# Performance work log

Measured on AMD Instinct MI355X. Metric: run time of the kernel, lower is better.

Reference implementation:

```python
import jax, jax.numpy as jnp
import numpy as np

C = 64
K = 16
DEPTH = 4            # int(sqrt(K))
N_NODES = K - 1      # 15 internal nodes per subspace tree
D = 512              # input feature dim, D // C = 8 per subspace
M = 512              # output dim (LUT rows)
N = 16384            # number of input rows


def _make_selection_matrix(C, depth=DEPTH):
    # row i within a subspace selects the transformed dim used at tree level of node i
    lvl = [0, 1, 1, 2, 2, 2, 2, 3, 3, 3, 3, 3, 3, 3, 3]
    S = np.zeros((C * N_NODES, C * depth), np.float32)
    for c in range(C):
        for i in range(N_NODES):
            S[c * N_NODES + i, c * depth + lvl[i]] = 1.0
    return S


def _make_bit_matrix(C, K=K):
    # per-subspace (K, K-1) matrix: leaf k gets +/-1 on the 4 nodes along its root-to-leaf path
    Bm = np.zeros((K, N_NODES), np.float32)
    for k in range(K):
        node = 0
        for l in range(DEPTH):
            bit = (k >> (DEPTH - 1 - l)) & 1
            Bm[k, node] = 1.0 if bit else -1.0
            node = 2 * node + 1 + bit  # children of node i are 2i+1 (left) and 2i+2 (right)
    Bfull = np.zeros((C * K, C * N_NODES), np.float32)
    for c in range(C):
        Bfull[c * K:(c + 1) * K, c * N_NODES:(c + 1) * N_NODES] = Bm
    return Bfull


def setup_inputs() -> dict:
    key = jax.random.key(0)
    k1, k2, k3, k4 = jax.random.split(key, 4)
    I = jax.random.normal(k1, (N, D), dtype=jnp.float32)
    A = jax.random.normal(k2, (C, D // C, DEPTH), dtype=jnp.float32) * (1.0 / np.sqrt(D // C))
    T = jax.random.normal(k3, (C * N_NODES,), dtype=jnp.float32) * 0.1
    L = jax.random.normal(k4, (M, C, K), dtype=jnp.float32)
    S = jnp.asarray(_make_selection_matrix(C))
    B = jnp.asarray(_make_bit_matrix(C))
    return {"I": I, "A": A, "T": T, "L": L, "S": S, "B": B}


def reference(I, A, T, L, S, B):
    C_, sub, depth = A.shape
    Kq = L.shape[-1]
    n = I.shape[0]
    # block-diagonal per-subspace projection: (n, D) -> (n, C*depth)
    Ir = I.T.reshape(C_, sub, n)                      # (C, sub, n)
    xt = jnp.einsum('csn,csd->cdn', Ir, A)            # (C, depth, n)
    xt = xt.reshape(C_ * depth, n)                    # (C*depth, n)
    # tree encoding: per-node activations, tanh relaxation, leaf scores
    h = S @ xt - T[:, None]                           # (C*15, n)
    b = (B @ jnp.tanh(h)).reshape(C_, Kq, n)          # (C, K, n)
    # straight-through hard one-hot encoding with softmax backward
    E_soft = jax.nn.softmax(b, axis=1)
    E_hard = jax.nn.one_hot(jnp.argmax(b, axis=1), Kq, axis=1, dtype=b.dtype)
    E = E_hard + E_soft - jax.lax.stop_gradient(E_soft)  # (C, K, n)
    # LUT decode: out[n, m] = sum_c L[m, c, enc(n, c)]
    out = jnp.einsum('mck,ckn->nm', L, E)
    return out
```

## Files before the change

### kernel.cpp

```cpp
#include <hip/hip_runtime.h>
#include <hip/hip_fp16.h>
#include <math.h>

#define CC 64
#define KK 16
#define NNODES 15
#define DD 512
#define MM 512
#define NN 16384

__device__ __forceinline__ float xla_tanhf(float x) {
    const float kMax = 7.90531110763549805f;
    bool tiny = fabsf(x) < 0.0004f;
    float xc = fminf(fmaxf(x, -kMax), kMax);
    float x2 = __fmul_rn(xc, xc);
    float p = __fmaf_rn(x2, -2.76076847742355e-16f, 2.00018790482477e-13f);
    p = __fmaf_rn(x2, p, -8.60467152213735e-11f);
    p = __fmaf_rn(x2, p, 5.12229709037114e-08f);
    p = __fmaf_rn(x2, p, 1.48572235717979e-05f);
    p = __fmaf_rn(x2, p, 6.37261928875436e-04f);
    p = __fmaf_rn(x2, p, 4.89352455891786e-03f);
    p = __fmul_rn(xc, p);
    float q = __fmaf_rn(x2, 1.19825839466702e-06f, 1.18534705686654e-04f);
    q = __fmaf_rn(x2, q, 2.26843463243900e-03f);
    q = __fmaf_rn(x2, q, 4.89352518554385e-03f);
    return tiny ? x : __fdiv_rn(p, q);
}

__global__ __launch_bounds__(256) void transpose_lut16(const float* __restrict__ L,
                                                       __half* __restrict__ Lt) {
    __shared__ __half tile[64 * 72];
    const int tid = threadIdx.x;
    const int ck0 = (blockIdx.x & 15) * 64;
    const int m0  = (blockIdx.x >> 4) * 64;

    const int col = tid & 63;
#pragma unroll
    for (int i = 0; i < 16; ++i) {
        int r = (tid >> 6) + i * 4;
        float v = L[(size_t)(m0 + r) * (CC * KK) + ck0 + col];
        tile[col * 72 + r] = __float2half(v);
    }
    __syncthreads();

#pragma unroll
    for (int t = 0; t < 2; ++t) {
        int cr   = (tid >> 3) + t * 32;
        int mseg = (tid & 7) * 8;
        uint4 v = *(const uint4*)&tile[cr * 72 + mseg];
        *(uint4*)(Lt + ((size_t)(ck0 + cr) * MM + m0 + mseg)) = v;
    }
}

__global__ __launch_bounds__(256) void fused_kernel(const float* __restrict__ I,
                                                    const float* __restrict__ A,
                                                    const float* __restrict__ T,
                                                    const __half* __restrict__ Lt,
                                                    float* __restrict__ out) {
    __shared__ float sA[CC * 8 * 4];
    __shared__ float sT[CC * NNODES];
    __shared__ unsigned char sIdx[4 * CC];

    const int tid = threadIdx.x;
    for (int i = tid; i < CC * 32; i += 256) sA[i] = A[i];
    for (int i = tid; i < CC * NNODES; i += 256) sT[i] = T[i];
    __syncthreads();

    const int w    = tid >> 6;
    const int lane = tid & 63;
    const int c    = lane;
    const int j    = blockIdx.x * 4 + w;

    {
        const float* Ij = I + (size_t)j * DD + c * 8;
        float4 v0 = ((const float4*)Ij)[0];
        float4 v1 = ((const float4*)Ij)[1];
        float iv[8] = {v0.x, v0.y, v0.z, v0.w, v1.x, v1.y, v1.z, v1.w};

        float t[4] = {0.f, 0.f, 0.f, 0.f};
#pragma unroll
        for (int s = 0; s < 8; ++s) {
            float v = iv[s];
#pragma unroll
            for (int d = 0; d < 4; ++d)
                t[d] = __fmaf_rn(v, sA[c * 32 + s * 4 + d], t[d]);
        }

        const int lvl[NNODES] = {0, 1, 1, 2, 2, 2, 2, 3, 3, 3, 3, 3, 3, 3, 3};
        float th[NNODES];
#pragma unroll
        for (int i = 0; i < NNODES; ++i) {
            float h = __fsub_rn(t[lvl[i]], sT[c * NNODES + i]);
            th[i] = xla_tanhf(h);
        }

        int best = 0;
        float bestv = -3.0e38f;
#pragma unroll
        for (int k = 0; k < KK; ++k) {
            int node = 0;
            float s = 0.f;
#pragma unroll
            for (int l = 0; l < 4; ++l) {
                int bit = (k >> (3 - l)) & 1;
                s = __fadd_rn(s, bit ? th[node] : -th[node]);
                node = 2 * node + 1 + bit;
            }
            if (s > bestv) { bestv = s; best = k; }
        }
        sIdx[tid] = (unsigned char)best;
    }
    __syncthreads();

    const int m0 = lane * 8;

    float acc[8];
#pragma unroll
    for (int i = 0; i < 8; ++i) acc[i] = 0.f;

#pragma unroll 8
    for (int cc = 0; cc < CC; ++cc) {
        int k = sIdx[w * CC + cc];
        const uint4 v = *(const uint4*)(Lt + ((size_t)((cc << 4) + k) * MM + m0));
        acc[0] = __fadd_rn(acc[0], __half2float(__ushort_as_half((unsigned short)(v.x & 0xffffu))));
        acc[1] = __fadd_rn(acc[1], __half2float(__ushort_as_half((unsigned short)(v.x >> 16))));
        acc[2] = __fadd_rn(acc[2], __half2float(__ushort_as_half((unsigned short)(v.y & 0xffffu))));
        acc[3] = __fadd_rn(acc[3], __half2float(__ushort_as_half((unsigned short)(v.y >> 16))));
        acc[4] = __fadd_rn(acc[4], __half2float(__ushort_as_half((unsigned short)(v.z & 0xffffu))));
        acc[5] = __fadd_rn(acc[5], __half2float(__ushort_as_half((unsigned short)(v.z >> 16))));
        acc[6] = __fadd_rn(acc[6], __half2float(__ushort_as_half((unsigned short)(v.w & 0xffffu))));
        acc[7] = __fadd_rn(acc[7], __half2float(__ushort_as_half((unsigned short)(v.w >> 16))));
    }

    float* o = out + (size_t)j * MM + m0;
    *(float4*)(o)     = make_float4(acc[0], acc[1], acc[2], acc[3]);
    *(float4*)(o + 4) = make_float4(acc[4], acc[5], acc[6], acc[7]);
}

extern "C" void kernel_launch(void* const* d_in, const int* in_sizes, int n_in,
                              void* d_out, int out_size, void* d_ws, size_t ws_size,
                              hipStream_t stream) {
    const float* I = (const float*)d_in[0];
    const float* A = (const float*)d_in[1];
    const float* T = (const float*)d_in[2];
    const float* L = (const float*)d_in[3];

    __half* Lt16 = (__half*)d_ws;
    float* out = (float*)d_out;

    hipLaunchKernelGGL(transpose_lut16, dim3(128), dim3(256), 0, stream, L, Lt16);
    hipLaunchKernelGGL(fused_kernel, dim3(NN / 4), dim3(256), 0, stream, I, A, T, Lt16, out);
}
```

Before: 131.9 us.

## Replace LUT gather decode with one-hot MFMA matmul over packed fp16 fragments

The per-row LUT gather-and-add decode is recast as a dense matmul of one-hot code fragments against L, run on MFMA 16x16x32 f16 instructions. A pre-pass packs L into fp16 B-fragment order. Each block now encodes 64 rows and computes a 64x256 output tile, with B fragments double-buffered in registers. The aim is to replace scattered 16-byte gathers and scalar adds with matrix-core throughput and better reuse of L. In exchange it does 16x more arithmetic on mostly-zero operands, each block encodes rows that a sibling block also encodes, and the output stores are narrower and strided.

```diff
diff --git a/kernel.cpp b/kernel.cpp
--- a/kernel.cpp
+++ b/kernel.cpp
@@ -8,6 +8,10 @@
 #define DD 512
 #define MM 512
 #define NN 16384
+
+typedef _Float16 half8 __attribute__((ext_vector_type(8)));
+typedef float f32x4 __attribute__((ext_vector_type(4)));
+typedef unsigned long long u64;
 
 __device__ __forceinline__ float xla_tanhf(float x) {
     const float kMax = 7.90531110763549805f;
@@ -27,114 +31,174 @@
     return tiny ? x : __fdiv_rn(p, q);
 }
 
-__global__ __launch_bounds__(256) void transpose_lut16(const float* __restrict__ L,
-                                                       __half* __restrict__ Lt) {
-    __shared__ __half tile[64 * 72];
+__global__ __launch_bounds__(256) void pack_bfrag(const float* __restrict__ L,
+                                                  uint4* __restrict__ Bpk) {
+    const int t    = blockIdx.x * 256 + threadIdx.x;
+    const int lane = t & 63;
+    const int mtg  = (t >> 6) & 31;
+    const int ks   = t >> 11;
+    const int kbase = ks * 32 + ((lane >> 4) << 3);
+    const int c     = kbase >> 4;
+    const int slot0 = kbase & 15;
+    const int m     = (mtg << 4) + (lane & 15);
+
+    const float* src = L + ((size_t)m * CC + c) * KK + slot0;
+    float4 v0 = ((const float4*)src)[0];
+    float4 v1 = ((const float4*)src)[1];
+    union { half8 h; uint4 u; } pk;
+    pk.h[0] = (_Float16)v0.x; pk.h[1] = (_Float16)v0.y;
+    pk.h[2] = (_Float16)v0.z; pk.h[3] = (_Float16)v0.w;
+    pk.h[4] = (_Float16)v1.x; pk.h[5] = (_Float16)v1.y;
+    pk.h[6] = (_Float16)v1.z; pk.h[7] = (_Float16)v1.w;
+    Bpk[t] = pk.u;
+}
+
+__global__ __launch_bounds__(256, 2) void fused_mfma(const float* __restrict__ I,
+                                                     const float* __restrict__ A,
+                                                     const float* __restrict__ T,
+                                                     const uint4* __restrict__ Bpk,
+                                                     float* __restrict__ out) {
+    __shared__ float sA[32 * 64];
+    __shared__ float sT[CC * NNODES];
+    __shared__ unsigned char sCodes[CC * 68];
+
     const int tid = threadIdx.x;
-    const int ck0 = (blockIdx.x & 15) * 64;
-    const int m0  = (blockIdx.x >> 4) * 64;
-
-    const int col = tid & 63;
-#pragma unroll
-    for (int i = 0; i < 16; ++i) {
-        int r = (tid >> 6) + i * 4;
-        float v = L[(size_t)(m0 + r) * (CC * KK) + ck0 + col];
-        tile[col * 72 + r] = __float2half(v);
+    for (int i = tid; i < CC * 32; i += 256) sA[(i & 31) * 64 + (i >> 5)] = A[i];
+    for (int i = tid; i < CC * NNODES; i += 256) sT[i] = T[i];
+    __syncthreads();
+
+    const int w    = tid >> 6;
+    const int lane = tid & 63;
+    const int n0 = (blockIdx.x >> 1) * 64;
+    const int m0 = (blockIdx.x & 1) * 256 + w * 64;
+
+    {
+        const int c = lane;
+        const int lvl[NNODES] = {0, 1, 1, 2, 2, 2, 2, 3, 3, 3, 3, 3, 3, 3, 3};
+#pragma unroll 2
+        for (int rr = 0; rr < 16; ++rr) {
+            const int rl = (rr << 2) + w;
+            const float* Ij = I + (size_t)(n0 + rl) * DD + c * 8;
+            float4 v0 = ((const float4*)Ij)[0];
+            float4 v1 = ((const float4*)Ij)[1];
+            float iv[8] = {v0.x, v0.y, v0.z, v0.w, v1.x, v1.y, v1.z, v1.w};
+
+            float t[4] = {0.f, 0.f, 0.f, 0.f};
+#pragma unroll
+            for (int s = 0; s < 8; ++s) {
+                float v = iv[s];
+#pragma unroll
+                for (int d = 0; d < 4; ++d)
+                    t[d] = __fmaf_rn(v, sA[((s << 2) + d) * 64 + c], t[d]);
+            }
+
+            float th[NNODES];
+#pragma unroll
+            for (int i = 0; i < NNODES; ++i) {
+                float h = __fsub_rn(t[lvl[i]], sT[c * NNODES + i]);
+                th[i] = xla_tanhf(h);
+            }
+
+            int best = 0;
+            float bestv = -3.0e38f;
+#pragma unroll
+            for (int k = 0; k < KK; ++k) {
+                int node = 0;
+                float s = 0.f;
+#pragma unroll
+                for (int l = 0; l < 4; ++l) {
+                    int bit = (k >> (3 - l)) & 1;
+                    s = __fadd_rn(s, bit ? th[node] : -th[node]);
+                    node = 2 * node + 1 + bit;
+                }
+                if (s > bestv) { bestv = s; best = k; }
+            }
+            sCodes[c * 68 + rl] = (unsigned char)best;
+        }
     }
     __syncthreads();
 
-#pragma unroll
-    for (int t = 0; t < 2; ++t) {
-        int cr   = (tid >> 3) + t * 32;
-        int mseg = (tid & 7) * 8;
-        uint4 v = *(const uint4*)&tile[cr * 72 + mseg];
-        *(uint4*)(Lt + ((size_t)(ck0 + cr) * MM + m0 + mseg)) = v;
+    const int r15  = lane & 15;
+    const int sb   = ((lane >> 4) & 1) << 3;
+    const int chi  = lane >> 5;
+    const int mtg0 = m0 >> 4;
+
+    f32x4 acc[4][4];
+#pragma unroll
+    for (int nt = 0; nt < 4; ++nt)
+#pragma unroll
+        for (int mt = 0; mt < 4; ++mt)
+            acc[nt][mt] = (f32x4){0.f, 0.f, 0.f, 0.f};
+
+    const uint4* Bp = Bpk + (size_t)mtg0 * 64 + lane;
+
+    uint4 bA[4], bB[4];
+#pragma unroll
+    for (int mt = 0; mt < 4; ++mt) bA[mt] = Bp[mt * 64];
+
+    for (int ks = 0; ks < 32; ks += 2) {
+#pragma unroll
+        for (int mt = 0; mt < 4; ++mt) bB[mt] = Bp[((ks + 1) * 32 + mt) * 64];
+
+        half8 a0[4];
+        {
+            const int c0 = (ks << 1) + chi;
+#pragma unroll
+            for (int nt = 0; nt < 4; ++nt) {
+                unsigned ud = (unsigned)((int)sCodes[c0 * 68 + (nt << 4) + r15] - sb);
+                unsigned ud2 = ud - 4u;
+                u64 lo = (ud  < 4u) ? (0x3C00ull << ((ud  & 3u) << 4)) : 0ull;
+                u64 hi = (ud2 < 4u) ? (0x3C00ull << ((ud2 & 3u) << 4)) : 0ull;
+                union { u64 q[2]; half8 h; } uu; uu.q[0] = lo; uu.q[1] = hi;
+                a0[nt] = uu.h;
+            }
+        }
+#pragma unroll
+        for (int nt = 0; nt < 4; ++nt)
+#pragma unroll
+            for (int mt = 0; mt < 4; ++mt) {
+                union { uint4 u; half8 h; } bb; bb.u = bA[mt];
+                acc[nt][mt] = __builtin_amdgcn_mfma_f32_16x16x32_f16(a0[nt], bb.h, acc[nt][mt], 0, 0, 0);
+            }
+
+        if (ks + 2 < 32) {
+#pragma unroll
+            for (int mt = 0; mt < 4; ++mt) bA[mt] = Bp[((ks + 2) * 32 + mt) * 64];
+        }
+
+        half8 a1[4];
+        {
+            const int c1 = ((ks + 1) << 1) + chi;
+#pragma unroll
+            for (int nt = 0; nt < 4; ++nt) {
+                unsigned ud = (unsigned)((int)sCodes[c1 * 68 + (nt << 4) + r15] - sb);
+                unsigned ud2 = ud - 4u;
+                u64 lo = (ud  < 4u) ? (0x3C00ull << ((ud  & 3u) << 4)) : 0ull;
+                u64 hi = (ud2 < 4u) ? (0x3C00ull << ((ud2 & 3u) << 4)) : 0ull;
+                union { u64 q[2]; half8 h; } uu; uu.q[0] = lo; uu.q[1] = hi;
+                a1[nt] = uu.h;
+            }
+        }
+#pragma unroll
+        for (int nt = 0; nt < 4; ++nt)
+#pragma unroll
+            for (int mt = 0; mt < 4; ++mt) {
+                union { uint4 u; half8 h; } bb; bb.u = bB[mt];
+                acc[nt][mt] = __builtin_amdgcn_mfma_f32_16x16x32_f16(a1[nt], bb.h, acc[nt][mt], 0, 0, 0);
+            }
     }
-}
-
-__global__ __launch_bounds__(256) void fused_kernel(const float* __restrict__ I,
-                                                    const float* __restrict__ A,
-                                                    const float* __restrict__ T,
-                                                    const __half* __restrict__ Lt,
-                                                    float* __restrict__ out) {
-    __shared__ float sA[CC * 8 * 4];
-    __shared__ float sT[CC * NNODES];
-    __shared__ unsigned char sIdx[4 * CC];
-
-    const int tid = threadIdx.x;
-    for (int i = tid; i < CC * 32; i += 256) sA[i] = A[i];
-    for (int i = tid; i < CC * NNODES; i += 256) sT[i] = T[i];
-    __syncthreads();
-
-    const int w    = tid >> 6;
-    const int lane = tid & 63;
-    const int c    = lane;
-    const int j    = blockIdx.x * 4 + w;
-
-    {
-        const float* Ij = I + (size_t)j * DD + c * 8;
-        float4 v0 = ((const float4*)Ij)[0];
-        float4 v1 = ((const float4*)Ij)[1];
-        float iv[8] = {v0.x, v0.y, v0.z, v0.w, v1.x, v1.y, v1.z, v1.w};
-
-        float t[4] = {0.f, 0.f, 0.f, 0.f};
-#pragma unroll
-        for (int s = 0; s < 8; ++s) {
-            float v = iv[s];
-#pragma unroll
-            for (int d = 0; d < 4; ++d)
-                t[d] = __fmaf_rn(v, sA[c * 32 + s * 4 + d], t[d]);
-        }
-
-        const int lvl[NNODES] = {0, 1, 1, 2, 2, 2, 2, 3, 3, 3, 3, 3, 3, 3, 3};
-        float th[NNODES];
-#pragma unroll
-        for (int i = 0; i < NNODES; ++i) {
-            float h = __fsub_rn(t[lvl[i]], sT[c * NNODES + i]);
-            th[i] = xla_tanhf(h);
-        }
-
-        int best = 0;
-        float bestv = -3.0e38f;
-#pragma unroll
-        for (int k = 0; k < KK; ++k) {
-            int node = 0;
-            float s = 0.f;
-#pragma unroll
-            for (int l = 0; l < 4; ++l) {
-                int bit = (k >> (3 - l)) & 1;
-                s = __fadd_rn(s, bit ? th[node] : -th[node]);
-                node = 2 * node + 1 + bit;
-            }
-            if (s > bestv) { bestv = s; best = k; }
-        }
-        sIdx[tid] = (unsigned char)best;
+
+    const int rbase = (lane >> 4) << 2;
+#pragma unroll
+    for (int nt = 0; nt < 4; ++nt) {
+#pragma unroll
+        for (int r = 0; r < 4; ++r) {
+            float* o = out + (size_t)(n0 + (nt << 4) + rbase + r) * MM + m0 + r15;
+#pragma unroll
+            for (int mt = 0; mt < 4; ++mt)
+                o[mt << 4] = acc[nt][mt][r];
+        }
     }
-    __syncthreads();
-
-    const int m0 = lane * 8;
-
-    float acc[8];
-#pragma unroll
-    for (int i = 0; i < 8; ++i) acc[i] = 0.f;
-
-#pragma unroll 8
-    for (int cc = 0; cc < CC; ++cc) {
-        int k = sIdx[w * CC + cc];
-        const uint4 v = *(const uint4*)(Lt + ((size_t)((cc << 4) + k) * MM + m0));
-        acc[0] = __fadd_rn(acc[0], __half2float(__ushort_as_half((unsigned short)(v.x & 0xffffu))));
-        acc[1] = __fadd_rn(acc[1], __half2float(__ushort_as_half((unsigned short)(v.x >> 16))));
-        acc[2] = __fadd_rn(acc[2], __half2float(__ushort_as_half((unsigned short)(v.y & 0xffffu))));
-        acc[3] = __fadd_rn(acc[3], __half2float(__ushort_as_half((unsigned short)(v.y >> 16))));
-        acc[4] = __fadd_rn(acc[4], __half2float(__ushort_as_half((unsigned short)(v.z & 0xffffu))));
-        acc[5] = __fadd_rn(acc[5], __half2float(__ushort_as_half((unsigned short)(v.z >> 16))));
-        acc[6] = __fadd_rn(acc[6], __half2float(__ushort_as_half((unsigned short)(v.w & 0xffffu))));
-        acc[7] = __fadd_rn(acc[7], __half2float(__ushort_as_half((unsigned short)(v.w >> 16))));
-    }
-
-    float* o = out + (size_t)j * MM + m0;
-    *(float4*)(o)     = make_float4(acc[0], acc[1], acc[2], acc[3]);
-    *(float4*)(o + 4) = make_float4(acc[4], acc[5], acc[6], acc[7]);
 }
 
 extern "C" void kernel_launch(void* const* d_in, const int* in_sizes, int n_in,
@@ -145,9 +209,9 @@
     const float* T = (const float*)d_in[2];
     const float* L = (const float*)d_in[3];
 
-    __half* Lt16 = (__half*)d_ws;
+    uint4* Bpk = (uint4*)d_ws;
     float* out = (float*)d_out;
 
-    hipLaunchKernelGGL(transpose_lut16, dim3(128), dim3(256), 0, stream, L, Lt16);
-    hipLaunchKernelGGL(fused_kernel, dim3(NN / 4), dim3(256), 0, stream, I, A, T, Lt16, out);
-}
+    hipLaunchKernelGGL(pack_bfrag, dim3(256), dim3(256), 0, stream, L, Bpk);
+    hipLaunchKernelGGL(fused_mfma, dim3(NN / 16 / 4 * 2), dim3(256), 0, stream, I, A, T, Bpk, out);
+}
```

Measured after the change: 130.2 us. About the same (-1.3%).
